# Kernel tuning notes

Measured on AMD Instinct MI355X. Metric: run time of the kernel, lower is better.

## Reference

```python
import jax, jax.numpy as jnp
import numpy as np

D = 1024
H = 16
HD = D // H
L = 2048
B = 1
MLP = 8192
ROPE_BASE = 10000.0
LN_EPS = 1e-5


def layer_norm(x):
    mu = jnp.mean(x, axis=-1, keepdims=True)
    var = jnp.var(x, axis=-1, keepdims=True)
    return (x - mu) / jnp.sqrt(var + LN_EPS)


def rope(x):
    # x: [B, H, L, HD]; non-traditional (rotate-half / NeoX style)
    half = HD // 2
    inv_freq = 1.0 / (ROPE_BASE ** (jnp.arange(0, half, dtype=jnp.float32) / half))
    pos = jnp.arange(x.shape[2], dtype=jnp.float32)
    ang = pos[:, None] * inv_freq[None, :]            # [L, half]
    cos, sin = jnp.cos(ang), jnp.sin(ang)
    x1, x2 = x[..., :half], x[..., half:]
    return jnp.concatenate([x1 * cos - x2 * sin, x2 * cos + x1 * sin], axis=-1).astype(x.dtype)


def setup_inputs() -> dict:
    key = jax.random.key(0)
    ks = jax.random.split(key, 5)
    x = jax.random.normal(ks[0], (B, L, D), dtype=jnp.float32)
    # causal additive mask
    neg = jnp.finfo(jnp.float32).min
    mask = jnp.where(jnp.tril(jnp.ones((L, L), dtype=bool)), 0.0, neg).astype(jnp.float32)
    W_attn = jax.random.normal(ks[1], (3 * D, D), dtype=jnp.float32) * (D ** -0.5)
    W_out = jax.random.normal(ks[2], (D, D), dtype=jnp.float32) * (D ** -0.5)
    W_ffp = jax.random.normal(ks[3], (MLP, D), dtype=jnp.float32) * (D ** -0.5)
    W_ffo = jax.random.normal(ks[4], (D, MLP // 2), dtype=jnp.float32) * ((MLP // 2) ** -0.5)
    return {"x": x, "mask": mask, "W_attn": W_attn, "W_out": W_out, "W_ffp": W_ffp, "W_ffo": W_ffo}


def block(x, mask, W_attn, W_out, W_ffp, W_ffo):
    b, l, d = x.shape
    scale = HD ** -0.5
    # attention branch
    xn = layer_norm(x)
    qkv = xn @ W_attn.T                                    # [B, L, 3D]
    q, k, v = jnp.split(qkv, 3, axis=-1)
    q = q.reshape(b, l, H, HD).transpose(0, 2, 1, 3)       # [B, H, L, HD]
    k = k.reshape(b, l, H, HD).transpose(0, 2, 1, 3)
    v = v.reshape(b, l, H, HD).transpose(0, 2, 1, 3)
    q = rope(q)
    k = rope(k)
    scores = jnp.einsum('bhqd,bhkd->bhqk', q * scale, k)   # [B, H, L, L]
    scores = scores + mask
    probs = jax.nn.softmax(scores.astype(jnp.float32), axis=-1).astype(scores.dtype)
    attn = jnp.einsum('bhqk,bhkd->bhqd', probs, v)
    attn = attn.transpose(0, 2, 1, 3).reshape(b, l, d)
    r = attn @ W_out.T
    h = x + r
    # SwiGLU MLP branch: split ff_proj output, swiglu(x2, x1) = silu(x2) * x1
    g = layer_norm(h) @ W_ffp.T                            # [B, L, MLP]
    x1, x2 = jnp.split(g, 2, axis=-1)
    mlp = (jax.nn.silu(x2) * x1) @ W_ffo.T
    return h + mlp


def reference(x, mask, W_attn, W_out, W_ffp, W_ffo):
    return block(x, mask, W_attn, W_out, W_ffp, W_ffo)
```

## Files before the change

kernel.cpp:

```cpp
#include <hip/hip_runtime.h>
#include <math.h>

#define DMODEL 1024
#define NHEAD  16
#define HDIM   64
#define SEQ    2048
#define MLPD   8192
#define HALF_MLP 4096
static constexpr float LN_EPS_C = 1e-5f;
#define NEG_BIG (-1e30f)
#define SM_SHIFT 16.0f

typedef short bf16x8 __attribute__((ext_vector_type(8)));
typedef float f32x4  __attribute__((ext_vector_type(4)));

__device__ __forceinline__ unsigned short f2b(float f) {
    unsigned int u = __float_as_uint(f);
    u = (u + 0x7FFFu + ((u >> 16) & 1u)) >> 16;
    return (unsigned short)u;
}
__device__ __forceinline__ float b2f(unsigned short h) {
    return __uint_as_float((unsigned int)h << 16);
}

__device__ __forceinline__ void async_copy16(const unsigned short* g, unsigned short* l) {
    __builtin_amdgcn_global_load_lds(
        (const __attribute__((address_space(1))) unsigned int*)(g),
        (__attribute__((address_space(3))) unsigned int*)(l),
        16, 0, 0);
}

__global__ void prep_all(const float* __restrict__ x,
                         const float* __restrict__ W_attn, const float* __restrict__ W_out,
                         const float* __restrict__ W_ffp,  const float* __restrict__ W_ffo,
                         unsigned short* __restrict__ xnb, float2* __restrict__ ct,
                         unsigned short* __restrict__ oa, unsigned short* __restrict__ ob,
                         unsigned short* __restrict__ oc, unsigned short* __restrict__ od) {
    const int bid = blockIdx.x;
    const int tid = threadIdx.x;
    if (bid < SEQ) {
        __shared__ float rs[256], rs2[256];
        float4 v = *(const float4*)(x + (size_t)bid * DMODEL + tid * 4);
        rs[tid]  = v.x + v.y + v.z + v.w;
        rs2[tid] = v.x * v.x + v.y * v.y + v.z * v.z + v.w * v.w;
        __syncthreads();
        for (int off = 128; off > 0; off >>= 1) {
            if (tid < off) { rs[tid] += rs[tid + off]; rs2[tid] += rs2[tid + off]; }
            __syncthreads();
        }
        float mu  = rs[0] * (1.0f / DMODEL);
        float var = rs2[0] * (1.0f / DMODEL) - mu * mu;
        float inv = rsqrtf(var + LN_EPS_C);
        ushort4 o;
        o.x = f2b((v.x - mu) * inv); o.y = f2b((v.y - mu) * inv);
        o.z = f2b((v.z - mu) * inv); o.w = f2b((v.w - mu) * inv);
        *(ushort4*)(xnb + (size_t)bid * DMODEL + tid * 4) = o;
    } else if (bid < SEQ + 256) {
        int idx = (bid - SEQ) * 256 + tid;
        int pos = idx >> 5, p = idx & 31;
        float invf = powf(10000.0f, -(float)p / 32.0f);
        float ang = (float)pos * invf;
        ct[idx] = make_float2(cosf(ang), sinf(ang));
    } else {
        const int n1 = 3 * DMODEL * DMODEL;
        const int n2 = n1 + DMODEL * DMODEL;
        const int n3 = n2 + MLPD * DMODEL;
        int i = ((bid - SEQ - 256) * 256 + tid) * 4;
        const float* src; unsigned short* dst; int off;
        if (i < n1)      { src = W_attn; dst = oa; off = i; }
        else if (i < n2) { src = W_out;  dst = ob; off = i - n1; }
        else if (i < n3) {
            src = W_ffp; off = i - n2;
            int row = off >> 10, col = off & 1023;
            int rp  = (row < HALF_MLP) ? (2 * row) : (2 * (row - HALF_MLP) + 1);
            float4 v = *(const float4*)(src + off);
            ushort4 o;
            o.x = f2b(v.x); o.y = f2b(v.y); o.z = f2b(v.z); o.w = f2b(v.w);
            *(ushort4*)(oc + ((size_t)rp << 10) + col) = o;
            return;
        }
        else             { src = W_ffo; dst = od; off = i - n3; }
        float4 v = *(const float4*)(src + off);
        ushort4 o;
        o.x = f2b(v.x); o.y = f2b(v.y); o.z = f2b(v.z); o.w = f2b(v.w);
        *(ushort4*)(dst + off) = o;
    }
}

__global__ void ln_red2(const float* __restrict__ p0, const float* __restrict__ p1,
                        const float* __restrict__ x, float* __restrict__ h,
                        unsigned short* __restrict__ xnb) {
    const int row = blockIdx.x;
    const int tid = threadIdx.x;
    __shared__ float rs[256], rs2[256];
    const size_t base = (size_t)row * DMODEL + tid * 4;
    float4 a = *(const float4*)(p0 + base);
    float4 b = *(const float4*)(p1 + base);
    float4 r = *(const float4*)(x + base);
    float4 v = { a.x + b.x + r.x, a.y + b.y + r.y, a.z + b.z + r.z, a.w + b.w + r.w };
    *(float4*)(h + base) = v;
    rs[tid]  = v.x + v.y + v.z + v.w;
    rs2[tid] = v.x * v.x + v.y * v.y + v.z * v.z + v.w * v.w;
    __syncthreads();
    for (int off = 128; off > 0; off >>= 1) {
        if (tid < off) { rs[tid] += rs[tid + off]; rs2[tid] += rs2[tid + off]; }
        __syncthreads();
    }
    float mu  = rs[0] * (1.0f / DMODEL);
    float var = rs2[0] * (1.0f / DMODEL) - mu * mu;
    float inv = rsqrtf(var + LN_EPS_C);
    ushort4 o;
    o.x = f2b((v.x - mu) * inv); o.y = f2b((v.y - mu) * inv);
    o.z = f2b((v.z - mu) * inv); o.w = f2b((v.w - mu) * inv);
    *(ushort4*)(xnb + base) = o;
}

__global__ __launch_bounds__(256, 2)
void gemm_qkv(const unsigned short* __restrict__ A, const unsigned short* __restrict__ B,
              const float2* __restrict__ ct,
              unsigned short* __restrict__ Qp, unsigned short* __restrict__ Kp,
              unsigned short* __restrict__ Vt) {
    __shared__ __align__(16) unsigned short U[4][2][128 * 32];
    __shared__ unsigned short St[4][16][72];
    const int tid  = threadIdx.x;
    const int lane = tid & 63;
    const int w    = tid >> 6;
    const int wm   = w >> 1;
    const int wn   = w & 1;
    const int m0   = blockIdx.y * 128;
    const int n0   = blockIdx.x * 128;

    f32x4 acc[4][4] = {};

    const int srow = lane >> 2;
    const int scg  = ((lane & 3) ^ ((lane >> 3) & 3)) * 8;
    const int fr   = lane & 15;
    const int quad = lane >> 4;
    const int rchunk = (quad ^ ((fr >> 1) & 3)) * 8;

#define QKV_STAGE(T)                                                          \
    {                                                                         \
        const int kk_ = (T) * 32;                                             \
        const int sl_ = (T) & 3;                                              \
        const unsigned short* ga_ = A + (size_t)(m0 + w * 32 + srow) * DMODEL + kk_ + scg; \
        const unsigned short* gb_ = B + (size_t)(n0 + w * 32 + srow) * DMODEL + kk_ + scg; \
        unsigned short* la_ = &U[sl_][0][(w * 32) * 32];                      \
        unsigned short* lb_ = &U[sl_][1][(w * 32) * 32];                      \
        async_copy16(ga_,               la_);                                 \
        async_copy16(ga_ + 16 * DMODEL, la_ + 16 * 32);                       \
        async_copy16(gb_,               lb_);                                 \
        async_copy16(gb_ + 16 * DMODEL, lb_ + 16 * 32);                       \
    }

    const int NT = DMODEL >> 5;
    QKV_STAGE(0)
    QKV_STAGE(1)
    asm volatile("s_waitcnt vmcnt(4)" ::: "memory");
    __builtin_amdgcn_s_barrier();

    for (int t = 0; t < NT; ++t) {
        if (t + 2 < NT) {
            QKV_STAGE(t + 2)
            asm volatile("s_waitcnt vmcnt(8)" ::: "memory");
        } else if (t + 1 < NT) {
            asm volatile("s_waitcnt vmcnt(4)" ::: "memory");
        } else {
            asm volatile("s_waitcnt vmcnt(0)" ::: "memory");
        }
        __builtin_amdgcn_s_barrier();
        __builtin_amdgcn_sched_barrier(0);

        const unsigned short* As_ = &U[t & 3][0][0];
        const unsigned short* Bs_ = &U[t & 3][1][0];
        bf16x8 af[4], bfr[4];
#pragma unroll
        for (int i = 0; i < 4; ++i)
            af[i] = *(const bf16x8*)&As_[(wm * 64 + i * 16 + fr) * 32 + rchunk];
#pragma unroll
        for (int j = 0; j < 4; ++j)
            bfr[j] = *(const bf16x8*)&Bs_[(wn * 64 + j * 16 + fr) * 32 + rchunk];

        __builtin_amdgcn_s_setprio(1);
#pragma unroll
        for (int i = 0; i < 4; ++i)
#pragma unroll
            for (int j = 0; j < 4; ++j)
                acc[i][j] = __builtin_amdgcn_mfma_f32_16x16x32_bf16(af[i], bfr[j], acc[i][j], 0, 0, 0);
        __builtin_amdgcn_s_setprio(0);
    }
#undef QKV_STAGE
    __syncthreads();

    const int erow   = (lane >> 4) * 4;
    const int ecol   = lane & 15;
    const int region = blockIdx.x >> 3;
    const int head   = ((n0 + wn * 64) >> 6) & 15;

    if (region == 2) {
        const int sbase = m0 + wm * 64;
        const int dl = lane >> 3;
        const int ch = (lane & 7) * 8;
#pragma unroll
        for (int j = 0; j < 4; ++j) {
#pragma unroll
            for (int i = 0; i < 4; ++i) {
                ushort4 o;
                o.x = f2b(acc[i][j][0]); o.y = f2b(acc[i][j][1]);
                o.z = f2b(acc[i][j][2]); o.w = f2b(acc[i][j][3]);
                *(ushort4*)&St[w][ecol][i * 16 + erow] = o;
            }
#pragma unroll
            for (int p = 0; p < 2; ++p) {
                const int dd = p * 8 + dl;
                bf16x8 v = *(const bf16x8*)&St[w][dd][ch];
                *(bf16x8*)(Vt + ((size_t)head * HDIM + j * 16 + dd) * SEQ + sbase + ch) = v;
            }
        }
    } else {
        unsigned short* P = region ? Kp : Qp;
        const float scale = region ? 1.0f : 0.125f;
        unsigned short* qb = &St[w][erow][0];
#pragma unroll
        for (int i = 0; i < 4; ++i) {
#pragma unroll
            for (int r = 0; r < 4; ++r) {
                const int rowg = m0 + wm * 64 + i * 16 + erow + r;
                const float2* crow = ct + (size_t)rowg * 32;
#pragma unroll
                for (int jj = 0; jj < 2; ++jj) {
                    const float2 cs = crow[jj * 16 + ecol];
                    const float x1 = acc[i][jj][r];
                    const float x2 = acc[i][jj + 2][r];
                    qb[jj * 16 + ecol]      = f2b((x1 * cs.x - x2 * cs.y) * scale);
                    qb[jj * 16 + ecol + 32] = f2b((x2 * cs.x + x1 * cs.y) * scale);
                }
                ushort4 o = *(const ushort4*)&qb[ecol * 4];
                *(ushort4*)(P + ((size_t)head * SEQ + rowg) * HDIM + ecol * 4) = o;
            }
        }
    }
}

__global__ __launch_bounds__(256, 2)
void gemm_mfma_sk(const unsigned short* __restrict__ A, const unsigned short* __restrict__ B,
                  float* __restrict__ P, int Ksub, int lda, int ldb, int ldc) {
    __shared__ __align__(16) unsigned short U[4][2][128 * 32];
    const int tid  = threadIdx.x;
    const int lane = tid & 63;
    const int w    = tid >> 6;
    const int wm   = w >> 1;
    const int wn   = w & 1;
    const int m0   = blockIdx.y * 128;
    const int n0   = blockIdx.x * 128;
    const int kb   = blockIdx.z * Ksub;

    f32x4 acc[4][4] = {};

    const int srow = lane >> 2;
    const int scg  = ((lane & 3) ^ ((lane >> 3) & 3)) * 8;
    const int fr   = lane & 15;
    const int quad = lane >> 4;
    const int rchunk = (quad ^ ((fr >> 1) & 3)) * 8;

#define SK_STAGE(T)                                                           \
    {                                                                         \
        const int kk_ = kb + (T) * 32;                                        \
        const int sl_ = (T) & 3;                                              \
        const unsigned short* ga_ = A + (size_t)(m0 + w * 32 + srow) * lda + kk_ + scg; \
        const unsigned short* gb_ = B + (size_t)(n0 + w * 32 + srow) * ldb + kk_ + scg; \
        unsigned short* la_ = &U[sl_][0][(w * 32) * 32];                      \
        unsigned short* lb_ = &U[sl_][1][(w * 32) * 32];                      \
        async_copy16(ga_,                    la_);                            \
        async_copy16(ga_ + 16 * (size_t)lda, la_ + 16 * 32);                  \
        async_copy16(gb_,                    lb_);                            \
        async_copy16(gb_ + 16 * (size_t)ldb, lb_ + 16 * 32);                  \
    }

    const int NT = Ksub >> 5;
    SK_STAGE(0)
    SK_STAGE(1)
    asm volatile("s_waitcnt vmcnt(4)" ::: "memory");
    __builtin_amdgcn_s_barrier();

    for (int t = 0; t < NT; ++t) {
        if (t + 2 < NT) {
            SK_STAGE(t + 2)
            asm volatile("s_waitcnt vmcnt(8)" ::: "memory");
        } else if (t + 1 < NT) {
            asm volatile("s_waitcnt vmcnt(4)" ::: "memory");
        } else {
            asm volatile("s_waitcnt vmcnt(0)" ::: "memory");
        }
        __builtin_amdgcn_s_barrier();
        __builtin_amdgcn_sched_barrier(0);

        const unsigned short* As_ = &U[t & 3][0][0];
        const unsigned short* Bs_ = &U[t & 3][1][0];
        bf16x8 af[4], bfr[4];
#pragma unroll
        for (int i = 0; i < 4; ++i)
            af[i] = *(const bf16x8*)&As_[(wm * 64 + i * 16 + fr) * 32 + rchunk];
#pragma unroll
        for (int j = 0; j < 4; ++j)
            bfr[j] = *(const bf16x8*)&Bs_[(wn * 64 + j * 16 + fr) * 32 + rchunk];

        __builtin_amdgcn_s_setprio(1);
#pragma unroll
        for (int i = 0; i < 4; ++i)
#pragma unroll
            for (int j = 0; j < 4; ++j)
                acc[i][j] = __builtin_amdgcn_mfma_f32_16x16x32_bf16(af[i], bfr[j], acc[i][j], 0, 0, 0);
        __builtin_amdgcn_s_setprio(0);
    }
#undef SK_STAGE

    float* Pp = P + (size_t)blockIdx.z * SEQ * ldc;
    const int erow = (lane >> 4) * 4;
    const int ecol = lane & 15;
#pragma unroll
    for (int i = 0; i < 4; ++i)
#pragma unroll
        for (int j = 0; j < 4; ++j) {
            const int colg = n0 + wn * 64 + j * 16 + ecol;
#pragma unroll
            for (int r = 0; r < 4; ++r) {
                const int rowg = m0 + wm * 64 + i * 16 + erow + r;
                Pp[(size_t)rowg * ldc + colg] = acc[i][j][r];
            }
        }
}

__global__ void reduce4_kernel(const float* __restrict__ p0, const float* __restrict__ p1,
                               const float* __restrict__ p2, const float* __restrict__ p3,
                               const float* __restrict__ res, float* __restrict__ out) {
    int i = (blockIdx.x * blockDim.x + threadIdx.x) * 4;
    float4 a = *(const float4*)(p0 + i);
    float4 b = *(const float4*)(p1 + i);
    float4 c = *(const float4*)(p2 + i);
    float4 d = *(const float4*)(p3 + i);
    float4 r = *(const float4*)(res + i);
    float4 o = { a.x + b.x + c.x + d.x + r.x, a.y + b.y + c.y + d.y + r.y,
                 a.z + b.z + c.z + d.z + r.z, a.w + b.w + c.w + d.w + r.w };
    *(float4*)(out + i) = o;
}

#define FT  32
#define FNT (DMODEL / FT)
__global__ __launch_bounds__(512, 2)
void gemm_ffp_silu_p(const unsigned short* __restrict__ A,
                     const unsigned short* __restrict__ B,
                     unsigned short* __restrict__ gact) {
    __shared__ __align__(16) unsigned short U[4][2][256 * 32];
    const int tid  = threadIdx.x;
    const int lane = tid & 63;
    const int w    = tid >> 6;
    const int wm   = w >> 2;
    const int wn   = w & 3;
    const int fr   = lane & 15;
    const int quad = lane >> 4;

    const int sid = (blockIdx.x & 7) * 32 + (blockIdx.x >> 3);
    const int tm  = sid & 7;
    const int tn  = sid >> 3;

    const unsigned short* Ag = A + (size_t)(tm * 256) * DMODEL;
    const unsigned short* Bg = B + (size_t)(tn * 256) * DMODEL;

    const int srow = tid >> 2;
    const int scg  = ((tid & 3) ^ ((tid >> 3) & 3)) * 8;
    unsigned short* lba = (unsigned short*)&U[0][0][0] + w * 512;
    unsigned short* lbb = (unsigned short*)&U[0][1][0] + w * 512;

    const int rchunk = (quad ^ ((fr >> 1) & 3)) * 8;

    f32x4 acc[8][4] = {};

#define FFP_STAGE(T)                                                          \
    {                                                                         \
        const int k0_ = (T) * FT;                                             \
        const int sl_ = (T) & 3;                                              \
        const unsigned short* ga_ = Ag + (size_t)srow * DMODEL + k0_ + scg;   \
        const unsigned short* gb_ = Bg + (size_t)srow * DMODEL + k0_ + scg;   \
        unsigned short* la_ = lba + sl_ * 16384;                              \
        unsigned short* lb_ = lbb + sl_ * 16384;                              \
        async_copy16(ga_,                la_);                                \
        async_copy16(ga_ + 128 * DMODEL, la_ + 4096);                         \
        async_copy16(gb_,                lb_);                                \
        async_copy16(gb_ + 128 * DMODEL, lb_ + 4096);                         \
    }

    FFP_STAGE(0)
    FFP_STAGE(1)
    asm volatile("s_waitcnt vmcnt(4)" ::: "memory");
    __builtin_amdgcn_s_barrier();

    for (int t = 0; t < FNT; ++t) {
        if (t + 2 < FNT) {
            FFP_STAGE(t + 2)
            asm volatile("s_waitcnt vmcnt(8)" ::: "memory");
        } else if (t + 1 < FNT) {
            asm volatile("s_waitcnt vmcnt(4)" ::: "memory");
        } else {
            asm volatile("s_waitcnt vmcnt(0)" ::: "memory");
        }
        __builtin_amdgcn_s_barrier();
        __builtin_amdgcn_sched_barrier(0);

        const unsigned short* As_ = &U[t & 3][0][0];
        const unsigned short* Bs_ = &U[t & 3][1][0];
        bf16x8 af[8], bf[4];
#pragma unroll
        for (int i = 0; i < 8; ++i)
            af[i] = *(const bf16x8*)&As_[(wm * 128 + i * 16 + fr) * 32 + rchunk];
#pragma unroll
        for (int j = 0; j < 4; ++j)
            bf[j] = *(const bf16x8*)&Bs_[(wn * 64 + j * 16 + fr) * 32 + rchunk];

        __builtin_amdgcn_s_setprio(1);
#pragma unroll
        for (int i = 0; i < 8; ++i)
#pragma unroll
            for (int j = 0; j < 4; ++j)
                acc[i][j] = __builtin_amdgcn_mfma_f32_16x16x32_bf16(af[i], bf[j], acc[i][j], 0, 0, 0);
        __builtin_amdgcn_s_setprio(0);
    }
#undef FFP_STAGE

    __syncthreads();
    typedef unsigned short StRow[40];
    StRow* Stw = reinterpret_cast<StRow*>(&U[0][0][0]) + (size_t)w * 128;

    const bool evn = (fr & 1) == 0;
#pragma unroll
    for (int i = 0; i < 8; ++i)
#pragma unroll
        for (int j = 0; j < 4; ++j)
#pragma unroll
            for (int r = 0; r < 4; ++r) {
                float own = acc[i][j][r];
                float oth = __shfl_xor(own, 1);
                if (evn) {
                    float sil = oth / (1.0f + __expf(-oth));
                    Stw[i * 16 + quad * 4 + r][j * 8 + (fr >> 1)] = f2b(sil * own);
                }
            }
    {
        const int growb = tm * 256 + wm * 128;
        const int colb  = tn * 128 + wn * 32;
#pragma unroll
        for (int p = 0; p < 2; ++p) {
            const int rl = p * 64 + lane;
            unsigned short* dst = gact + (size_t)(growb + rl) * HALF_MLP + colb;
            bf16x8 v0 = *(const bf16x8*)&Stw[rl][0];
            bf16x8 v1 = *(const bf16x8*)&Stw[rl][8];
            bf16x8 v2 = *(const bf16x8*)&Stw[rl][16];
            bf16x8 v3 = *(const bf16x8*)&Stw[rl][24];
            *(bf16x8*)(dst + 0)  = v0;
            *(bf16x8*)(dst + 8)  = v1;
            *(bf16x8*)(dst + 16) = v2;
            *(bf16x8*)(dst + 24) = v3;
        }
    }
}

__global__ __launch_bounds__(256)
void fattn_blk(const unsigned short* __restrict__ Qp,
               const unsigned short* __restrict__ Kp,
               const unsigned short* __restrict__ Vt,
               unsigned short* __restrict__ out) {
    __shared__ unsigned short Ks[2][64][64];
    __shared__ unsigned short Vs[2][64][64];
    __shared__ unsigned short Ps[4][16][72];
    const int tid  = threadIdx.x;
    const int lane = tid & 63;
    const int w    = tid >> 6;
    const int fr   = lane & 15;
    const int quad = lane >> 4;

    const int f    = blockIdx.x;
    const int head = ((f & 7) << 1) | ((f >> 3) & 1);
    const int ub   = f >> 4;
    const int qb   = (ub & 1) ? (31 - (ub >> 1)) : (ub >> 1);
    const int m0   = qb * 64 + w * 16;

    const unsigned short* Qg = Qp + (size_t)head * SEQ * HDIM;
    const unsigned short* Kg = Kp + (size_t)head * SEQ * HDIM;
    const unsigned short* Vg = Vt + (size_t)head * HDIM * SEQ;

    const int rA = (w << 3) + (lane >> 3);
    const int cg = ((lane & 7) ^ ((lane >> 3) & 7)) << 3;

    bf16x8 qf[2];
#pragma unroll
    for (int kk = 0; kk < 2; ++kk)
        qf[kk] = *(const bf16x8*)(Qg + (size_t)(m0 + fr) * HDIM + kk * 32 + quad * 8);

    bf16x8 ones;
#pragma unroll
    for (int e = 0; e < 8; ++e) ones[e] = (short)0x3F80;

    f32x4 accO[4] = {};
    f32x4 accL = {};

    const int ntiles = qb + 1;

    {
        const unsigned short* gk = Kg + (size_t)rA * HDIM + cg;
        unsigned short* dk = &Ks[0][w << 3][0];
        async_copy16(gk, dk);
        async_copy16(gk + 32 * HDIM, dk + 32 * 64);
        const unsigned short* gv = Vg + (size_t)rA * SEQ + cg;
        unsigned short* dv = &Vs[0][w << 3][0];
        async_copy16(gv, dv);
        async_copy16(gv + 32 * SEQ, dv + 32 * 64);
    }
    __syncthreads();

    int cur = 0;
    for (int t = 0; t < ntiles; ++t) {
        if (t + 1 < ntiles) {
            const int j1 = (t + 1) * 64;
            const unsigned short* gk = Kg + (size_t)(j1 + rA) * HDIM + cg;
            unsigned short* dk = &Ks[cur ^ 1][w << 3][0];
            async_copy16(gk, dk);
            async_copy16(gk + 32 * HDIM, dk + 32 * 64);
            const unsigned short* gv = Vg + (size_t)rA * SEQ + j1 + cg;
            unsigned short* dv = &Vs[cur ^ 1][w << 3][0];
            async_copy16(gv, dv);
            async_copy16(gv + 32 * SEQ, dv + 32 * 64);
        }

        const int j0 = t * 64;
        f32x4 accS[4] = {};
#pragma unroll
        for (int kk = 0; kk < 2; ++kk) {
#pragma unroll
            for (int j = 0; j < 4; ++j) {
                bf16x8 kf = *(const bf16x8*)
                    &Ks[cur][j * 16 + fr][(((kk << 2) + quad) ^ (fr & 7)) << 3];
                accS[j] = __builtin_amdgcn_mfma_f32_16x16x32_bf16(qf[kk], kf, accS[j], 0, 0, 0);
            }
        }

        if (t == ntiles - 1) {
#pragma unroll
            for (int j = 0; j < 4; ++j)
#pragma unroll
                for (int r = 0; r < 4; ++r)
                    if (j0 + j * 16 + fr > m0 + quad * 4 + r) accS[j][r] = NEG_BIG;
        }

#pragma unroll
        for (int j = 0; j < 4; ++j)
#pragma unroll
            for (int r = 0; r < 4; ++r)
                Ps[w][quad * 4 + r][j * 16 + fr] = f2b(__expf(accS[j][r] - SM_SHIFT));

#pragma unroll
        for (int kk = 0; kk < 2; ++kk) {
            bf16x8 pf = *(const bf16x8*)&Ps[w][fr][kk * 32 + quad * 8];
            accL = __builtin_amdgcn_mfma_f32_16x16x32_bf16(pf, ones, accL, 0, 0, 0);
#pragma unroll
            for (int j = 0; j < 4; ++j) {
                bf16x8 vf = *(const bf16x8*)
                    &Vs[cur][j * 16 + fr][(((kk << 2) + quad) ^ (fr & 7)) << 3];
                accO[j] = __builtin_amdgcn_mfma_f32_16x16x32_bf16(pf, vf, accO[j], 0, 0, 0);
            }
        }

        __syncthreads();
        cur ^= 1;
    }

#pragma unroll
    for (int r = 0; r < 4; ++r) {
        const float inv = 1.0f / accL[r];
        const int qrow = m0 + quad * 4 + r;
#pragma unroll
        for (int j = 0; j < 4; ++j)
            out[(size_t)qrow * DMODEL + head * HDIM + j * 16 + fr] = f2b(accO[j][r] * inv);
    }
}

extern "C" void kernel_launch(void* const* d_in, const int* in_sizes, int n_in,
                              void* d_out, int out_size, void* d_ws, size_t ws_size,
                              hipStream_t stream) {
    const float* x      = (const float*)d_in[0];
    const float* W_attn = (const float*)d_in[2];
    const float* W_out  = (const float*)d_in[3];
    const float* W_ffp  = (const float*)d_in[4];
    const float* W_ffo  = (const float*)d_in[5];
    float* out = (float*)d_out;

    char* wsb = (char*)d_ws;
    unsigned short* wb_attn = (unsigned short*)(wsb);
    unsigned short* wb_out  = (unsigned short*)(wsb + (6u  << 20));
    unsigned short* wb_ffp  = (unsigned short*)(wsb + (8u  << 20));
    unsigned short* wb_ffo  = (unsigned short*)(wsb + (24u << 20));
    float*          h       = (float*)(wsb + (32u << 20));
    unsigned short* xnb     = (unsigned short*)(wsb + (40u << 20));
    unsigned short* attnb   = (unsigned short*)(wsb + (44u << 20));
    unsigned short* gact    = (unsigned short*)(wsb + (48u << 20));
    unsigned short* Qp      = (unsigned short*)(wsb + (64u << 20));
    unsigned short* Kp      = (unsigned short*)(wsb + (68u << 20));
    unsigned short* Vt      = (unsigned short*)(wsb + (72u << 20));
    float*          wout_p  = (float*)(wsb + (76u << 20));
    float2*         ct      = (float2*)(wsb + (92u << 20));
    float*          ffo_p   = (float*)(wsb + (64u << 20));

    {
        int f2b_blocks = (3 * DMODEL * DMODEL + DMODEL * DMODEL + MLPD * DMODEL
                          + DMODEL * HALF_MLP) / 4 / 256;
        prep_all<<<SEQ + 256 + f2b_blocks, 256, 0, stream>>>(
            x, W_attn, W_out, W_ffp, W_ffo, xnb, ct,
            wb_attn, wb_out, wb_ffp, wb_ffo);
    }

    gemm_qkv<<<dim3(3 * DMODEL / 128, SEQ / 128), 256, 0, stream>>>(
        xnb, wb_attn, ct, Qp, Kp, Vt);

    fattn_blk<<<512, 256, 0, stream>>>(Qp, Kp, Vt, attnb);

    gemm_mfma_sk<<<dim3(DMODEL / 128, SEQ / 128, 2), 256, 0, stream>>>(
        attnb, wb_out, wout_p, DMODEL / 2, DMODEL, DMODEL, DMODEL);

    ln_red2<<<SEQ, 256, 0, stream>>>(wout_p, wout_p + (size_t)SEQ * DMODEL, x, h, xnb);

    gemm_ffp_silu_p<<<256, 512, 0, stream>>>(xnb, wb_ffp, gact);

    gemm_mfma_sk<<<dim3(DMODEL / 128, SEQ / 128, 4), 256, 0, stream>>>(
        gact, wb_ffo, ffo_p, HALF_MLP / 4, HALF_MLP, HALF_MLP, DMODEL);

    reduce4_kernel<<<SEQ * DMODEL / 4 / 256, 256, 0, stream>>>(
        ffo_p, ffo_p + (size_t)SEQ * DMODEL, ffo_p + 2 * (size_t)SEQ * DMODEL,
        ffo_p + 3 * (size_t)SEQ * DMODEL, h, out);
}
```

Before: 280.9 us.

## Deepen attention K/V prefetch to a 4-slot ring with explicit vmcnt waits

The flash-attention kernel now keeps two K/V tiles in flight ahead of compute instead of one, using a four-slot shared-memory ring. The per-iteration __syncthreads is replaced with targeted s_waitcnt vmcnt counts plus a single s_barrier, and wave priority is raised around the MFMA sections. The goal is to hide global load latency better and cut barrier overhead. In exchange it doubles K/V shared memory, which may reduce occupancy, and it depends on the async copy count per stage matching the hard-coded vmcnt values.

Measured after the change: 279.0 us. Within noise of the previous version (-0.7%).

```diff
diff --git a/kernel.cpp b/kernel.cpp
--- a/kernel.cpp
+++ b/kernel.cpp
@@ -468,8 +468,8 @@
                const unsigned short* __restrict__ Kp,
                const unsigned short* __restrict__ Vt,
                unsigned short* __restrict__ out) {
-    __shared__ unsigned short Ks[2][64][64];
-    __shared__ unsigned short Vs[2][64][64];
+    __shared__ unsigned short Ks[4][64][64];
+    __shared__ unsigned short Vs[4][64][64];
     __shared__ unsigned short Ps[4][16][72];
     const int tid  = threadIdx.x;
     const int lane = tid & 63;
@@ -504,43 +504,55 @@
 
     const int ntiles = qb + 1;
 
-    {
-        const unsigned short* gk = Kg + (size_t)rA * HDIM + cg;
-        unsigned short* dk = &Ks[0][w << 3][0];
-        async_copy16(gk, dk);
-        async_copy16(gk + 32 * HDIM, dk + 32 * 64);
-        const unsigned short* gv = Vg + (size_t)rA * SEQ + cg;
-        unsigned short* dv = &Vs[0][w << 3][0];
-        async_copy16(gv, dv);
-        async_copy16(gv + 32 * SEQ, dv + 32 * 64);
-    }
-    __syncthreads();
-
-    int cur = 0;
+#define FA_STAGE(T)                                                           \
+    {                                                                         \
+        const int j_  = (T) * 64;                                             \
+        const int sl_ = (T) & 3;                                              \
+        const unsigned short* gk = Kg + (size_t)(j_ + rA) * HDIM + cg;        \
+        unsigned short* dk = &Ks[sl_][w << 3][0];                             \
+        async_copy16(gk, dk);                                                 \
+        async_copy16(gk + 32 * HDIM, dk + 32 * 64);                           \
+        const unsigned short* gv = Vg + (size_t)rA * SEQ + j_ + cg;           \
+        unsigned short* dv = &Vs[sl_][w << 3][0];                             \
+        async_copy16(gv, dv);                                                 \
+        async_copy16(gv + 32 * SEQ, dv + 32 * 64);                            \
+    }
+
+    FA_STAGE(0)
+    if (ntiles > 1) {
+        FA_STAGE(1)
+        asm volatile("s_waitcnt vmcnt(4)" ::: "memory");
+    } else {
+        asm volatile("s_waitcnt vmcnt(0)" ::: "memory");
+    }
+    __builtin_amdgcn_s_barrier();
+
     for (int t = 0; t < ntiles; ++t) {
-        if (t + 1 < ntiles) {
-            const int j1 = (t + 1) * 64;
-            const unsigned short* gk = Kg + (size_t)(j1 + rA) * HDIM + cg;
-            unsigned short* dk = &Ks[cur ^ 1][w << 3][0];
-            async_copy16(gk, dk);
-            async_copy16(gk + 32 * HDIM, dk + 32 * 64);
-            const unsigned short* gv = Vg + (size_t)rA * SEQ + j1 + cg;
-            unsigned short* dv = &Vs[cur ^ 1][w << 3][0];
-            async_copy16(gv, dv);
-            async_copy16(gv + 32 * SEQ, dv + 32 * 64);
-        }
+        if (t + 2 < ntiles) {
+            FA_STAGE(t + 2)
+            asm volatile("s_waitcnt vmcnt(8)" ::: "memory");
+        } else if (t + 1 < ntiles) {
+            asm volatile("s_waitcnt vmcnt(4)" ::: "memory");
+        } else {
+            asm volatile("s_waitcnt vmcnt(0)" ::: "memory");
+        }
+        __builtin_amdgcn_s_barrier();
+        __builtin_amdgcn_sched_barrier(0);
 
         const int j0 = t * 64;
+        const int sl = t & 3;
         f32x4 accS[4] = {};
+        __builtin_amdgcn_s_setprio(1);
 #pragma unroll
         for (int kk = 0; kk < 2; ++kk) {
 #pragma unroll
             for (int j = 0; j < 4; ++j) {
                 bf16x8 kf = *(const bf16x8*)
-                    &Ks[cur][j * 16 + fr][(((kk << 2) + quad) ^ (fr & 7)) << 3];
+                    &Ks[sl][j * 16 + fr][(((kk << 2) + quad) ^ (fr & 7)) << 3];
                 accS[j] = __builtin_amdgcn_mfma_f32_16x16x32_bf16(qf[kk], kf, accS[j], 0, 0, 0);
             }
         }
+        __builtin_amdgcn_s_setprio(0);
 
         if (t == ntiles - 1) {
 #pragma unroll
@@ -556,6 +568,7 @@
             for (int r = 0; r < 4; ++r)
                 Ps[w][quad * 4 + r][j * 16 + fr] = f2b(__expf(accS[j][r] - SM_SHIFT));
 
+        __builtin_amdgcn_s_setprio(1);
 #pragma unroll
         for (int kk = 0; kk < 2; ++kk) {
             bf16x8 pf = *(const bf16x8*)&Ps[w][fr][kk * 32 + quad * 8];
@@ -563,14 +576,13 @@
 #pragma unroll
             for (int j = 0; j < 4; ++j) {
                 bf16x8 vf = *(const bf16x8*)
-                    &Vs[cur][j * 16 + fr][(((kk << 2) + quad) ^ (fr & 7)) << 3];
+                    &Vs[sl][j * 16 + fr][(((kk << 2) + quad) ^ (fr & 7)) << 3];
                 accO[j] = __builtin_amdgcn_mfma_f32_16x16x32_bf16(pf, vf, accO[j], 0, 0, 0);
             }
         }
-
-        __syncthreads();
-        cur ^= 1;
-    }
+        __builtin_amdgcn_s_setprio(0);
+    }
+#undef FA_STAGE
 
 #pragma unroll
     for (int r = 0; r < 4; ++r) {
```
